# Optimization experiments

Hardware: AMD Instinct MI355X
Metric: run time of the kernel (lower is better)

## Reference

```python
import jax, jax.numpy as jnp
import numpy as np

E, T, DIN, DOUT = 8, 32768, 1024, 4096


def setup_inputs() -> dict:
    key = jax.random.key(0)
    k1, k2, k3 = jax.random.split(key, 3)
    input = jax.random.normal(k1, (T, DIN), dtype=jnp.float32)
    weight = jax.random.normal(k2, (E, DOUT, DIN), dtype=jnp.float32) * 0.02
    bias = jax.random.normal(k3, (E, DOUT), dtype=jnp.float32) * 0.02
    # balanced routing: 4096 tokens per expert, sums to T
    num_experts_per_token = jnp.full((E,), T // E, dtype=jnp.int64)
    return {"input": input, "weight": weight, "bias": bias,
            "num_experts_per_token": num_experts_per_token}


def reference(input, weight, bias, num_experts_per_token):
    # counts are routing metadata -> static (mirrors .tolist() in torch)
    counts = np.asarray(num_experts_per_token)
    offsets = np.concatenate([[0], np.cumsum(counts)])  # [E+1]
    num_experts = weight.shape[0]
    outs = []
    for i in range(num_experts):  # fixed small loop over experts (grouped GEMM)
        xi = input[offsets[i]:offsets[i + 1]]          # [n_i, DIN]
        yi = xi @ weight[i].T + bias[i]                # [n_i, DOUT]
        outs.append(yi)
    return jnp.concatenate(outs, axis=0)               # [T, DOUT]
```

## Files before the change

kernel.cpp:

```cpp
#include <hip/hip_runtime.h>
#include <hip/hip_bf16.h>


#define DEVFN __device__ __forceinline__

constexpr int E_    = 8;
constexpr int T_    = 32768;
constexpr int DIN_  = 1024;
constexpr int DOUT_ = 4096;

typedef __attribute__((ext_vector_type(8))) __bf16 bf16x8;
typedef __attribute__((ext_vector_type(4))) float  f32x4;
typedef __attribute__((ext_vector_type(8))) short  s16x8;

DEVFN unsigned short f2bf(float x) {
  unsigned u = __builtin_bit_cast(unsigned, x);
  u += 0x7fffu + ((u >> 16) & 1u);
  return (unsigned short)(u >> 16);
}

DEVFN long long expert_offset(const void* cnts, int e) {
  const int* c32 = (const int*)cnts;
  long long s = 0;
  for (int i = 0; i < E_; ++i) s += c32[i];
  if (s == (long long)T_) {
    long long o = 0;
    for (int i = 0; i < e; ++i) o += c32[i];
    return o;
  }
  const long long* c64 = (const long long*)cnts;
  long long o = 0;
  for (int i = 0; i < e; ++i) o += c64[i];
  return o;
}

__global__ __launch_bounds__(256) void cvt_kernel(const float* __restrict__ in,
                                                  unsigned short* __restrict__ out,
                                                  int n4) {
  int i = blockIdx.x * 256 + threadIdx.x;
  if (i >= n4) return;
  const float4 f = reinterpret_cast<const float4*>(in)[i];
  ushort4 h;
  h.x = f2bf(f.x); h.y = f2bf(f.y); h.z = f2bf(f.z); h.w = f2bf(f.w);
  reinterpret_cast<ushort4*>(out)[i] = h;
}

__global__ __launch_bounds__(512, 2) void gemm2_kernel(const unsigned short* __restrict__ wa,
                                                       const unsigned short* __restrict__ wb,
                                                       const float* __restrict__ bias,
                                                       const void* __restrict__ counts,
                                                       float* __restrict__ out) {
  __shared__ __align__(16) unsigned char lds[2][2][32768];

  const int tid  = threadIdx.x;
  const int lane = tid & 63;
  const int wid  = tid >> 6;
  const int wm = wid >> 2, wn = wid & 3;

  const int bid = blockIdx.x;
  const int sid = (bid & 7) * 256 + (bid >> 3);
  const int e  = sid >> 8;
  const int t  = sid & 255;
  const int tm = t >> 4, tn = t & 15;

  const long long off = expert_offset(counts, e);
  const unsigned short* wat = wa + (off + (long long)tm * 256) * DIN_;
  const unsigned short* wbt = wb + ((long long)(e * DOUT_ + tn * 256)) * DIN_;

  int goff[4], loff[4];
#pragma unroll
  for (int rd = 0; rd < 4; ++rd) {
    const int chunk = rd * 512 + tid;
    const int r = chunk >> 3, c = chunk & 7;
    goff[rd] = r * DIN_ + (c ^ (r & 7)) * 8;
    loff[rd] = chunk * 16;
  }
  auto stage = [&](const unsigned short* g, unsigned char* l) {
#pragma unroll
    for (int rd = 0; rd < 4; ++rd)
      __builtin_amdgcn_global_load_lds(
          (const __attribute__((address_space(1))) void*)(g + goff[rd]),
          (__attribute__((address_space(3))) void*)(l + loff[rd]), 16, 0, 0);
  };

  const int rsel = lane & 15, hi = lane >> 4;
  int lp[2];
  lp[0] = rsel * 128 + (((hi)     ^ (rsel & 7)) << 4);
  lp[1] = rsel * 128 + (((4 + hi) ^ (rsel & 7)) << 4);

  bf16x8 a[4][2];
  bf16x8 b[2][2][2];
  f32x4  acc[8][4] = {};

  auto quad = [&](int am0, int q) {
#pragma unroll
    for (int mf = 0; mf < 4; ++mf)
#pragma unroll
      for (int j = 0; j < 2; ++j)
#pragma unroll
        for (int kk = 0; kk < 2; ++kk)
          acc[am0 + mf][q * 2 + j] = __builtin_amdgcn_mfma_f32_16x16x32_bf16(
              a[mf][kk], b[q][j][kk], acc[am0 + mf][q * 2 + j], 0, 0, 0);
  };

  const int abase = wm * 128 * 128;
  const int bbase = wn * 64 * 128;

  auto ktile = [&](unsigned char* Ab, unsigned char* Bb,
                   const unsigned short* pfa, const unsigned short* pfb,
                   bool pf, int nend) {
#pragma unroll
    for (int mf = 0; mf < 4; ++mf)
#pragma unroll
      for (int kk = 0; kk < 2; ++kk)
        a[mf][kk] = *(const bf16x8*)(Ab + abase + mf * 2048 + lp[kk]);
#pragma unroll
    for (int j = 0; j < 2; ++j)
#pragma unroll
      for (int kk = 0; kk < 2; ++kk)
        b[0][j][kk] = *(const bf16x8*)(Bb + bbase + j * 2048 + lp[kk]);
    __builtin_amdgcn_s_barrier();
    asm volatile("s_waitcnt lgkmcnt(0)" ::: "memory");
    __builtin_amdgcn_sched_barrier(0);
    __builtin_amdgcn_s_setprio(1);
    quad(0, 0);
    __builtin_amdgcn_s_setprio(0);
    __builtin_amdgcn_s_barrier();

#pragma unroll
    for (int j = 0; j < 2; ++j)
#pragma unroll
      for (int kk = 0; kk < 2; ++kk)
        b[1][j][kk] = *(const bf16x8*)(Bb + bbase + (32 + j * 16) * 128 + lp[kk]);
    __builtin_amdgcn_s_barrier();
    asm volatile("s_waitcnt lgkmcnt(0)" ::: "memory");
    __builtin_amdgcn_sched_barrier(0);
    __builtin_amdgcn_s_setprio(1);
    quad(0, 1);
    __builtin_amdgcn_s_setprio(0);
    __builtin_amdgcn_s_barrier();

#pragma unroll
    for (int mf = 0; mf < 4; ++mf)
#pragma unroll
      for (int kk = 0; kk < 2; ++kk)
        a[mf][kk] = *(const bf16x8*)(Ab + abase + 8192 + mf * 2048 + lp[kk]);
    if (pf) stage(pfb, Bb);
    __builtin_amdgcn_s_barrier();
    asm volatile("s_waitcnt lgkmcnt(0)" ::: "memory");
    __builtin_amdgcn_sched_barrier(0);
    __builtin_amdgcn_s_setprio(1);
    quad(4, 1);
    __builtin_amdgcn_s_setprio(0);
    __builtin_amdgcn_s_barrier();

    if (pf) stage(pfa, Ab);
    __builtin_amdgcn_s_barrier();
    __builtin_amdgcn_sched_barrier(0);
    __builtin_amdgcn_s_setprio(1);
    quad(4, 0);
    __builtin_amdgcn_s_setprio(0);
    if (nend == 8)      asm volatile("s_waitcnt vmcnt(8)" ::: "memory");
    else if (nend == 0) asm volatile("s_waitcnt vmcnt(0)" ::: "memory");
    __builtin_amdgcn_s_barrier();
  };

  stage(wat,      &lds[0][0][0]);
  stage(wbt,      &lds[0][1][0]);
  stage(wat + 64, &lds[1][0][0]);
  stage(wbt + 64, &lds[1][1][0]);
  asm volatile("s_waitcnt vmcnt(8)" ::: "memory");
  __builtin_amdgcn_s_barrier();

  for (int it = 0; it < 7; ++it) {
    const int k0 = 2 * it;
    ktile(&lds[0][0][0], &lds[0][1][0], wat + (k0 + 2) * 64, wbt + (k0 + 2) * 64, true, 8);
    ktile(&lds[1][0][0], &lds[1][1][0], wat + (k0 + 3) * 64, wbt + (k0 + 3) * 64, true, 8);
  }
  ktile(&lds[0][0][0], &lds[0][1][0], nullptr, nullptr, false, 0);
  ktile(&lds[1][0][0], &lds[1][1][0], nullptr, nullptr, false, -1);

  const long long orow0 = off + (long long)tm * 256 + wm * 128;
  const int ocol0 = tn * 256 + wn * 64;
  const int rlo = hi * 4;
  const int c15 = rsel;
#pragma unroll
  for (int nf = 0; nf < 4; ++nf) {
    const int ncol = ocol0 + nf * 16 + c15;
    const float bv = bias[e * DOUT_ + ncol];
#pragma unroll
    for (int am = 0; am < 8; ++am) {
      const int rl = (am >> 2) * 64 + (am & 3) * 16 + rlo;
#pragma unroll
      for (int j = 0; j < 4; ++j)
        out[(orow0 + rl + j) * (long long)DOUT_ + ncol] = acc[am][nf][j] + bv;
    }
  }
}

__global__ __launch_bounds__(256) void gemm_fb_kernel(const float* __restrict__ Af,
                                                      const float* __restrict__ Bf,
                                                      const float* __restrict__ bias,
                                                      const void* __restrict__ counts,
                                                      float* __restrict__ out) {
  constexpr int RS = 144;
  constexpr int BBASE = 128 * RS;
  __shared__ __align__(16) unsigned char lds[2 * 128 * RS];

  const int tid  = threadIdx.x;
  const int lane = tid & 63;
  const int wid  = tid >> 6;
  const int wm = wid >> 1, wn = wid & 1;

  const int bid = blockIdx.x;
  const int e  = bid >> 10;
  const int t  = bid & 1023;
  const int tm = t >> 5, tn = t & 31;

  const long long off = expert_offset(counts, e);
  const long long rowA0 = off + (long long)tm * 128;
  const int n0 = tn * 128;

  f32x4 acc[4][4] = {};

  for (int kt = 0; kt < DIN_ / 64; ++kt) {
    const int k0 = kt * 64;
#pragma unroll
    for (int rd = 0; rd < 8; ++rd) {
      const int chunk = rd * 256 + tid;
      const int c2 = chunk & 1023;
      const int r  = c2 >> 3;
      const int c  = c2 & 7;
      const float* src =
          (rd < 4) ? (Af + (rowA0 + r) * (long long)DIN_ + (k0 + c * 8))
                   : (Bf + ((long long)(e * DOUT_ + n0 + r)) * DIN_ + (k0 + c * 8));
      const float4 f0 = *reinterpret_cast<const float4*>(src);
      const float4 f1 = *reinterpret_cast<const float4*>(src + 4);
      s16x8 v;
      v[0] = (short)f2bf(f0.x); v[1] = (short)f2bf(f0.y);
      v[2] = (short)f2bf(f0.z); v[3] = (short)f2bf(f0.w);
      v[4] = (short)f2bf(f1.x); v[5] = (short)f2bf(f1.y);
      v[6] = (short)f2bf(f1.z); v[7] = (short)f2bf(f1.w);
      *reinterpret_cast<s16x8*>(&lds[((rd < 4) ? 0 : BBASE) + r * RS + (c << 4)]) = v;
    }
    __syncthreads();
#pragma unroll
    for (int kk = 0; kk < 2; ++kk) {
      const int rs = lane & 15;
      const int cs = kk * 4 + (lane >> 4);
      bf16x8 af[4], bfr[4];
#pragma unroll
      for (int mf = 0; mf < 4; ++mf)
        af[mf] = *reinterpret_cast<const bf16x8*>(&lds[(wm * 64 + mf * 16 + rs) * RS + (cs << 4)]);
#pragma unroll
      for (int nf = 0; nf < 4; ++nf)
        bfr[nf] = *reinterpret_cast<const bf16x8*>(&lds[BBASE + (wn * 64 + nf * 16 + rs) * RS + (cs << 4)]);
#pragma unroll
      for (int mf = 0; mf < 4; ++mf)
#pragma unroll
        for (int nf = 0; nf < 4; ++nf)
          acc[mf][nf] = __builtin_amdgcn_mfma_f32_16x16x32_bf16(af[mf], bfr[nf], acc[mf][nf], 0, 0, 0);
    }
    __syncthreads();
  }

  const long long orow0 = off + (long long)tm * 128 + wm * 64;
  const int ocol0 = n0 + wn * 64;
  const int rlo = (lane >> 4) * 4;
  const int c15 = lane & 15;
#pragma unroll
  for (int nf = 0; nf < 4; ++nf) {
    const int n = ocol0 + nf * 16 + c15;
    const float bv = bias[e * DOUT_ + n];
#pragma unroll
    for (int mf = 0; mf < 4; ++mf) {
      const long long mrow = orow0 + mf * 16 + rlo;
#pragma unroll
      for (int j = 0; j < 4; ++j)
        out[(mrow + j) * (long long)DOUT_ + n] = acc[mf][nf][j] + bv;
    }
  }
}

extern "C" void kernel_launch(void* const* d_in, const int* in_sizes, int n_in,
                              void* d_out, int out_size, void* d_ws, size_t ws_size,
                              hipStream_t stream) {
  const float* input  = (const float*)d_in[0];
  const float* weight = (const float*)d_in[1];
  const float* bias   = (const float*)d_in[2];
  const void*  counts = (const void*)d_in[3];
  float* out = (float*)d_out;

  const size_t nA = (size_t)T_ * DIN_;
  const size_t nW = (size_t)E_ * DOUT_ * DIN_;
  const size_t need = (nA + nW) * sizeof(unsigned short);

  if (ws_size >= need) {
    unsigned short* wa = (unsigned short*)d_ws;
    unsigned short* wb = wa + nA;
    cvt_kernel<<<dim3((unsigned)(nA / 4 / 256)), dim3(256), 0, stream>>>(input, wa, (int)(nA / 4));
    cvt_kernel<<<dim3((unsigned)(nW / 4 / 256)), dim3(256), 0, stream>>>(weight, wb, (int)(nW / 4));
    gemm2_kernel<<<dim3(2048), dim3(512), 0, stream>>>(wa, wb, bias, counts, out);
  } else {
    gemm_fb_kernel<<<dim3(E_ * 32 * 32), dim3(256), 0, stream>>>(input, weight, bias, counts, out);
  }
}
```

Before: 403.8 us.

## Switch grouped GEMM to 256x128 tiles with BK=32 and 4-wave blocks

Replaces the 512-thread 256x256 tile kernel (BK=64, 128 KB LDS) with a 256-thread 256x128 tile kernel using BK=32 and 48 KB double-buffered LDS. The pipeline is restructured into per-k-tile phases that stage the next B tile and the A tile two steps ahead, with a new XOR swizzle for the narrower rows. This aims to raise occupancy and shorten the prologue and epilogue per block. In exchange the tile is smaller and k-steps shorter, so each block reuses less data and there are more barriers per unit of work.

```diff
diff --git a/kernel.cpp b/kernel.cpp
--- a/kernel.cpp
+++ b/kernel.cpp
@@ -8,6 +8,7 @@
 constexpr int T_    = 32768;
 constexpr int DIN_  = 1024;
 constexpr int DOUT_ = 4096;
+constexpr int NKT   = 32;
 
 typedef __attribute__((ext_vector_type(8))) __bf16 bf16x8;
 typedef __attribute__((ext_vector_type(4))) float  f32x4;
@@ -45,155 +46,124 @@
   reinterpret_cast<ushort4*>(out)[i] = h;
 }
 
-__global__ __launch_bounds__(512, 2) void gemm2_kernel(const unsigned short* __restrict__ wa,
+__global__ __launch_bounds__(256, 2) void gemm3_kernel(const unsigned short* __restrict__ wa,
                                                        const unsigned short* __restrict__ wb,
                                                        const float* __restrict__ bias,
                                                        const void* __restrict__ counts,
                                                        float* __restrict__ out) {
-  __shared__ __align__(16) unsigned char lds[2][2][32768];
+  __shared__ __align__(16) unsigned char lds[2][24576];
 
   const int tid  = threadIdx.x;
   const int lane = tid & 63;
   const int wid  = tid >> 6;
-  const int wm = wid >> 2, wn = wid & 3;
+  const int wm = wid >> 1, wn = wid & 1;
 
   const int bid = blockIdx.x;
-  const int sid = (bid & 7) * 256 + (bid >> 3);
-  const int e  = sid >> 8;
-  const int t  = sid & 255;
-  const int tm = t >> 4, tn = t & 15;
+  const int sid = (bid & 7) * 512 + (bid >> 3);
+  const int e  = sid >> 9;
+  const int t  = sid & 511;
+  const int tm = t >> 5, tn = t & 31;
 
   const long long off = expert_offset(counts, e);
   const unsigned short* wat = wa + (off + (long long)tm * 256) * DIN_;
-  const unsigned short* wbt = wb + ((long long)(e * DOUT_ + tn * 256)) * DIN_;
-
-  int goff[4], loff[4];
+  const unsigned short* wbt = wb + ((long long)(e * DOUT_ + tn * 128)) * DIN_;
+
+  int gA[4], gB[2];
 #pragma unroll
   for (int rd = 0; rd < 4; ++rd) {
-    const int chunk = rd * 512 + tid;
-    const int r = chunk >> 3, c = chunk & 7;
-    goff[rd] = r * DIN_ + (c ^ (r & 7)) * 8;
-    loff[rd] = chunk * 16;
-  }
-  auto stage = [&](const unsigned short* g, unsigned char* l) {
+    const int chunk = rd * 256 + tid;
+    const int r = chunk >> 2, c = chunk & 3;
+    gA[rd] = r * DIN_ + ((c ^ ((r >> 1) & 3)) << 3);
+  }
+#pragma unroll
+  for (int rd = 0; rd < 2; ++rd) {
+    const int chunk = rd * 256 + tid;
+    const int r = chunk >> 2, c = chunk & 3;
+    gB[rd] = r * DIN_ + ((c ^ ((r >> 1) & 3)) << 3);
+  }
+  auto stageA = [&](int kt, int buf) {
 #pragma unroll
     for (int rd = 0; rd < 4; ++rd)
       __builtin_amdgcn_global_load_lds(
-          (const __attribute__((address_space(1))) void*)(g + goff[rd]),
-          (__attribute__((address_space(3))) void*)(l + loff[rd]), 16, 0, 0);
+          (const __attribute__((address_space(1))) void*)(wat + kt * 32 + gA[rd]),
+          (__attribute__((address_space(3))) void*)(&lds[buf][(rd * 256 + tid) * 16]), 16, 0, 0);
   };
-
-  const int rsel = lane & 15, hi = lane >> 4;
-  int lp[2];
-  lp[0] = rsel * 128 + (((hi)     ^ (rsel & 7)) << 4);
-  lp[1] = rsel * 128 + (((4 + hi) ^ (rsel & 7)) << 4);
-
-  bf16x8 a[4][2];
-  bf16x8 b[2][2][2];
+  auto stageB = [&](int kt, int buf) {
+#pragma unroll
+    for (int rd = 0; rd < 2; ++rd)
+      __builtin_amdgcn_global_load_lds(
+          (const __attribute__((address_space(1))) void*)(wbt + kt * 32 + gB[rd]),
+          (__attribute__((address_space(3))) void*)(&lds[buf][16384 + (rd * 256 + tid) * 16]), 16, 0, 0);
+  };
+
+  const int rsel = lane & 15, g = lane >> 4;
+  const int swz = ((g ^ ((rsel >> 1) & 3)) << 4);
+  int laoff[8], lboff[4];
+#pragma unroll
+  for (int mf = 0; mf < 8; ++mf) laoff[mf] = (wm * 128 + mf * 16 + rsel) * 64 + swz;
+#pragma unroll
+  for (int nf = 0; nf < 4; ++nf) lboff[nf] = 16384 + (wn * 64 + nf * 16 + rsel) * 64 + swz;
+
+  bf16x8 a[8], b[2];
   f32x4  acc[8][4] = {};
 
-  auto quad = [&](int am0, int q) {
-#pragma unroll
-    for (int mf = 0; mf < 4; ++mf)
-#pragma unroll
-      for (int j = 0; j < 2; ++j)
-#pragma unroll
-        for (int kk = 0; kk < 2; ++kk)
-          acc[am0 + mf][q * 2 + j] = __builtin_amdgcn_mfma_f32_16x16x32_bf16(
-              a[mf][kk], b[q][j][kk], acc[am0 + mf][q * 2 + j], 0, 0, 0);
-  };
-
-  const int abase = wm * 128 * 128;
-  const int bbase = wn * 64 * 128;
-
-  auto ktile = [&](unsigned char* Ab, unsigned char* Bb,
-                   const unsigned short* pfa, const unsigned short* pfb,
-                   bool pf, int nend) {
-#pragma unroll
-    for (int mf = 0; mf < 4; ++mf)
-#pragma unroll
-      for (int kk = 0; kk < 2; ++kk)
-        a[mf][kk] = *(const bf16x8*)(Ab + abase + mf * 2048 + lp[kk]);
-#pragma unroll
-    for (int j = 0; j < 2; ++j)
-#pragma unroll
-      for (int kk = 0; kk < 2; ++kk)
-        b[0][j][kk] = *(const bf16x8*)(Bb + bbase + j * 2048 + lp[kk]);
+  stageA(0, 0);
+  stageB(0, 0);
+  stageA(1, 1);
+  asm volatile("s_waitcnt vmcnt(4)" ::: "memory");
+  __builtin_amdgcn_s_barrier();
+
+  for (int kt = 0; kt < NKT; ++kt) {
+    unsigned char* Ab = &lds[kt & 1][0];
+#pragma unroll
+    for (int mf = 0; mf < 8; ++mf) a[mf] = *(const bf16x8*)(Ab + laoff[mf]);
+    b[0] = *(const bf16x8*)(Ab + lboff[0]);
+    b[1] = *(const bf16x8*)(Ab + lboff[1]);
+    if (kt < NKT - 1) stageB(kt + 1, (kt + 1) & 1);
     __builtin_amdgcn_s_barrier();
     asm volatile("s_waitcnt lgkmcnt(0)" ::: "memory");
     __builtin_amdgcn_sched_barrier(0);
     __builtin_amdgcn_s_setprio(1);
-    quad(0, 0);
+#pragma unroll
+    for (int nf = 0; nf < 2; ++nf)
+#pragma unroll
+      for (int mf = 0; mf < 8; ++mf)
+        acc[mf][nf] = __builtin_amdgcn_mfma_f32_16x16x32_bf16(a[mf], b[nf], acc[mf][nf], 0, 0, 0);
     __builtin_amdgcn_s_setprio(0);
     __builtin_amdgcn_s_barrier();
 
-#pragma unroll
-    for (int j = 0; j < 2; ++j)
-#pragma unroll
-      for (int kk = 0; kk < 2; ++kk)
-        b[1][j][kk] = *(const bf16x8*)(Bb + bbase + (32 + j * 16) * 128 + lp[kk]);
+    b[0] = *(const bf16x8*)(Ab + lboff[2]);
+    b[1] = *(const bf16x8*)(Ab + lboff[3]);
+    if (kt < NKT - 2) stageA(kt + 2, kt & 1);
     __builtin_amdgcn_s_barrier();
     asm volatile("s_waitcnt lgkmcnt(0)" ::: "memory");
     __builtin_amdgcn_sched_barrier(0);
     __builtin_amdgcn_s_setprio(1);
-    quad(0, 1);
+#pragma unroll
+    for (int nf = 0; nf < 2; ++nf)
+#pragma unroll
+      for (int mf = 0; mf < 8; ++mf)
+        acc[mf][2 + nf] = __builtin_amdgcn_mfma_f32_16x16x32_bf16(a[mf], b[nf], acc[mf][2 + nf], 0, 0, 0);
     __builtin_amdgcn_s_setprio(0);
-    __builtin_amdgcn_s_barrier();
-
-#pragma unroll
-    for (int mf = 0; mf < 4; ++mf)
-#pragma unroll
-      for (int kk = 0; kk < 2; ++kk)
-        a[mf][kk] = *(const bf16x8*)(Ab + abase + 8192 + mf * 2048 + lp[kk]);
-    if (pf) stage(pfb, Bb);
-    __builtin_amdgcn_s_barrier();
-    asm volatile("s_waitcnt lgkmcnt(0)" ::: "memory");
-    __builtin_amdgcn_sched_barrier(0);
-    __builtin_amdgcn_s_setprio(1);
-    quad(4, 1);
-    __builtin_amdgcn_s_setprio(0);
-    __builtin_amdgcn_s_barrier();
-
-    if (pf) stage(pfa, Ab);
-    __builtin_amdgcn_s_barrier();
-    __builtin_amdgcn_sched_barrier(0);
-    __builtin_amdgcn_s_setprio(1);
-    quad(4, 0);
-    __builtin_amdgcn_s_setprio(0);
-    if (nend == 8)      asm volatile("s_waitcnt vmcnt(8)" ::: "memory");
-    else if (nend == 0) asm volatile("s_waitcnt vmcnt(0)" ::: "memory");
-    __builtin_amdgcn_s_barrier();
-  };
-
-  stage(wat,      &lds[0][0][0]);
-  stage(wbt,      &lds[0][1][0]);
-  stage(wat + 64, &lds[1][0][0]);
-  stage(wbt + 64, &lds[1][1][0]);
-  asm volatile("s_waitcnt vmcnt(8)" ::: "memory");
-  __builtin_amdgcn_s_barrier();
-
-  for (int it = 0; it < 7; ++it) {
-    const int k0 = 2 * it;
-    ktile(&lds[0][0][0], &lds[0][1][0], wat + (k0 + 2) * 64, wbt + (k0 + 2) * 64, true, 8);
-    ktile(&lds[1][0][0], &lds[1][1][0], wat + (k0 + 3) * 64, wbt + (k0 + 3) * 64, true, 8);
-  }
-  ktile(&lds[0][0][0], &lds[0][1][0], nullptr, nullptr, false, 0);
-  ktile(&lds[1][0][0], &lds[1][1][0], nullptr, nullptr, false, -1);
+    if (kt < NKT - 2)       asm volatile("s_waitcnt vmcnt(4)" ::: "memory");
+    else if (kt == NKT - 2) asm volatile("s_waitcnt vmcnt(0)" ::: "memory");
+    __builtin_amdgcn_s_barrier();
+  }
 
   const long long orow0 = off + (long long)tm * 256 + wm * 128;
-  const int ocol0 = tn * 256 + wn * 64;
-  const int rlo = hi * 4;
+  const int ocol0 = tn * 128 + wn * 64;
+  const int rlo = g * 4;
   const int c15 = rsel;
 #pragma unroll
   for (int nf = 0; nf < 4; ++nf) {
     const int ncol = ocol0 + nf * 16 + c15;
     const float bv = bias[e * DOUT_ + ncol];
 #pragma unroll
-    for (int am = 0; am < 8; ++am) {
-      const int rl = (am >> 2) * 64 + (am & 3) * 16 + rlo;
+    for (int mf = 0; mf < 8; ++mf) {
+      const long long mrow = orow0 + mf * 16 + rlo;
 #pragma unroll
       for (int j = 0; j < 4; ++j)
-        out[(orow0 + rl + j) * (long long)DOUT_ + ncol] = acc[am][nf][j] + bv;
+        out[(mrow + j) * (long long)DOUT_ + ncol] = acc[mf][nf][j] + bv;
     }
   }
 }
@@ -300,7 +270,7 @@
     unsigned short* wb = wa + nA;
     cvt_kernel<<<dim3((unsigned)(nA / 4 / 256)), dim3(256), 0, stream>>>(input, wa, (int)(nA / 4));
     cvt_kernel<<<dim3((unsigned)(nW / 4 / 256)), dim3(256), 0, stream>>>(weight, wb, (int)(nW / 4));
-    gemm2_kernel<<<dim3(2048), dim3(512), 0, stream>>>(wa, wb, bias, counts, out);
+    gemm3_kernel<<<dim3(4096), dim3(256), 0, stream>>>(wa, wb, bias, counts, out);
   } else {
     gemm_fb_kernel<<<dim3(E_ * 32 * 32), dim3(256), 0, stream>>>(input, weight, bias, counts, out);
   }
```

Result: slower. 461.9 us (+14.4%).

## Make GEMM persistent with 256 blocks and prefetch next tile across tile boundaries

Applied to the files above, without the earlier changes.

The grouped GEMM kernel becomes persistent. It launches 256 blocks, one per CU, and each block walks 8 output tiles of its expert. During the last k-steps of the current tile it prefetches the first k-tiles of the next tile, which hides the pipeline fill and drain between tiles. It also seeds the accumulators with the bias instead of adding it at store time, and removes some of the barriers and lgkmcnt waits inside the k-loop. The costs are a fixed tile assignment with no load balancing and possible LDS race risk from the reduced synchronisation.

```diff
diff --git a/kernel.cpp b/kernel.cpp
--- a/kernel.cpp
+++ b/kernel.cpp
@@ -45,7 +45,7 @@
   reinterpret_cast<ushort4*>(out)[i] = h;
 }
 
-__global__ __launch_bounds__(512, 2) void gemm2_kernel(const unsigned short* __restrict__ wa,
+__global__ __launch_bounds__(512, 2) void gemm4_kernel(const unsigned short* __restrict__ wa,
                                                        const unsigned short* __restrict__ wb,
                                                        const float* __restrict__ bias,
                                                        const void* __restrict__ counts,
@@ -57,114 +57,55 @@
   const int wid  = tid >> 6;
   const int wm = wid >> 2, wn = wid & 3;
 
-  const int bid = blockIdx.x;
-  const int sid = (bid & 7) * 256 + (bid >> 3);
-  const int e  = sid >> 8;
-  const int t  = sid & 255;
-  const int tm = t >> 4, tn = t & 15;
+  const int p = blockIdx.x;
+  const int e = p & 7;
+  const int q = p >> 3;
 
   const long long off = expert_offset(counts, e);
-  const unsigned short* wat = wa + (off + (long long)tm * 256) * DIN_;
-  const unsigned short* wbt = wb + ((long long)(e * DOUT_ + tn * 256)) * DIN_;
-
-  int goff[4], loff[4];
+  const unsigned short* wae = wa + off * (long long)DIN_;
+  const unsigned short* wbe = wb + (long long)e * DOUT_ * DIN_;
+  const float* be = bias + e * DOUT_;
+
+  int goff[4];
 #pragma unroll
   for (int rd = 0; rd < 4; ++rd) {
     const int chunk = rd * 512 + tid;
     const int r = chunk >> 3, c = chunk & 7;
-    goff[rd] = r * DIN_ + (c ^ (r & 7)) * 8;
-    loff[rd] = chunk * 16;
+    goff[rd] = r * DIN_ + ((c ^ (r & 7)) << 3);
   }
   auto stage = [&](const unsigned short* g, unsigned char* l) {
 #pragma unroll
     for (int rd = 0; rd < 4; ++rd)
       __builtin_amdgcn_global_load_lds(
           (const __attribute__((address_space(1))) void*)(g + goff[rd]),
-          (__attribute__((address_space(3))) void*)(l + loff[rd]), 16, 0, 0);
+          (__attribute__((address_space(3))) void*)(l + (rd * 512 + tid) * 16), 16, 0, 0);
   };
 
   const int rsel = lane & 15, hi = lane >> 4;
   int lp[2];
   lp[0] = rsel * 128 + (((hi)     ^ (rsel & 7)) << 4);
   lp[1] = rsel * 128 + (((4 + hi) ^ (rsel & 7)) << 4);
+  const int abase = wm * 128 * 128;
+  const int bbase = wn * 64 * 128;
 
   bf16x8 a[4][2];
   bf16x8 b[2][2][2];
-  f32x4  acc[8][4] = {};
-
-  auto quad = [&](int am0, int q) {
+  f32x4  acc[8][4];
+
+  auto quad = [&](int am0, int qn) {
 #pragma unroll
     for (int mf = 0; mf < 4; ++mf)
 #pragma unroll
       for (int j = 0; j < 2; ++j)
 #pragma unroll
         for (int kk = 0; kk < 2; ++kk)
-          acc[am0 + mf][q * 2 + j] = __builtin_amdgcn_mfma_f32_16x16x32_bf16(
-              a[mf][kk], b[q][j][kk], acc[am0 + mf][q * 2 + j], 0, 0, 0);
+          acc[am0 + mf][qn * 2 + j] = __builtin_amdgcn_mfma_f32_16x16x32_bf16(
+              a[mf][kk], b[qn][j][kk], acc[am0 + mf][qn * 2 + j], 0, 0, 0);
   };
 
-  const int abase = wm * 128 * 128;
-  const int bbase = wn * 64 * 128;
-
-  auto ktile = [&](unsigned char* Ab, unsigned char* Bb,
-                   const unsigned short* pfa, const unsigned short* pfb,
-                   bool pf, int nend) {
-#pragma unroll
-    for (int mf = 0; mf < 4; ++mf)
-#pragma unroll
-      for (int kk = 0; kk < 2; ++kk)
-        a[mf][kk] = *(const bf16x8*)(Ab + abase + mf * 2048 + lp[kk]);
-#pragma unroll
-    for (int j = 0; j < 2; ++j)
-#pragma unroll
-      for (int kk = 0; kk < 2; ++kk)
-        b[0][j][kk] = *(const bf16x8*)(Bb + bbase + j * 2048 + lp[kk]);
-    __builtin_amdgcn_s_barrier();
-    asm volatile("s_waitcnt lgkmcnt(0)" ::: "memory");
-    __builtin_amdgcn_sched_barrier(0);
-    __builtin_amdgcn_s_setprio(1);
-    quad(0, 0);
-    __builtin_amdgcn_s_setprio(0);
-    __builtin_amdgcn_s_barrier();
-
-#pragma unroll
-    for (int j = 0; j < 2; ++j)
-#pragma unroll
-      for (int kk = 0; kk < 2; ++kk)
-        b[1][j][kk] = *(const bf16x8*)(Bb + bbase + (32 + j * 16) * 128 + lp[kk]);
-    __builtin_amdgcn_s_barrier();
-    asm volatile("s_waitcnt lgkmcnt(0)" ::: "memory");
-    __builtin_amdgcn_sched_barrier(0);
-    __builtin_amdgcn_s_setprio(1);
-    quad(0, 1);
-    __builtin_amdgcn_s_setprio(0);
-    __builtin_amdgcn_s_barrier();
-
-#pragma unroll
-    for (int mf = 0; mf < 4; ++mf)
-#pragma unroll
-      for (int kk = 0; kk < 2; ++kk)
-        a[mf][kk] = *(const bf16x8*)(Ab + abase + 8192 + mf * 2048 + lp[kk]);
-    if (pf) stage(pfb, Bb);
-    __builtin_amdgcn_s_barrier();
-    asm volatile("s_waitcnt lgkmcnt(0)" ::: "memory");
-    __builtin_amdgcn_sched_barrier(0);
-    __builtin_amdgcn_s_setprio(1);
-    quad(4, 1);
-    __builtin_amdgcn_s_setprio(0);
-    __builtin_amdgcn_s_barrier();
-
-    if (pf) stage(pfa, Ab);
-    __builtin_amdgcn_s_barrier();
-    __builtin_amdgcn_sched_barrier(0);
-    __builtin_amdgcn_s_setprio(1);
-    quad(4, 0);
-    __builtin_amdgcn_s_setprio(0);
-    if (nend == 8)      asm volatile("s_waitcnt vmcnt(8)" ::: "memory");
-    else if (nend == 0) asm volatile("s_waitcnt vmcnt(0)" ::: "memory");
-    __builtin_amdgcn_s_barrier();
-  };
-
+  int tm = q >> 3, tn = q & 7;
+  const unsigned short* wat = wae + (long long)tm * 256 * DIN_;
+  const unsigned short* wbt = wbe + (long long)tn * 256 * DIN_;
   stage(wat,      &lds[0][0][0]);
   stage(wbt,      &lds[0][1][0]);
   stage(wat + 64, &lds[1][0][0]);
@@ -172,29 +113,84 @@
   asm volatile("s_waitcnt vmcnt(8)" ::: "memory");
   __builtin_amdgcn_s_barrier();
 
-  for (int it = 0; it < 7; ++it) {
-    const int k0 = 2 * it;
-    ktile(&lds[0][0][0], &lds[0][1][0], wat + (k0 + 2) * 64, wbt + (k0 + 2) * 64, true, 8);
-    ktile(&lds[1][0][0], &lds[1][1][0], wat + (k0 + 3) * 64, wbt + (k0 + 3) * 64, true, 8);
-  }
-  ktile(&lds[0][0][0], &lds[0][1][0], nullptr, nullptr, false, 0);
-  ktile(&lds[1][0][0], &lds[1][1][0], nullptr, nullptr, false, -1);
-
-  const long long orow0 = off + (long long)tm * 256 + wm * 128;
-  const int ocol0 = tn * 256 + wn * 64;
-  const int rlo = hi * 4;
-  const int c15 = rsel;
-#pragma unroll
-  for (int nf = 0; nf < 4; ++nf) {
-    const int ncol = ocol0 + nf * 16 + c15;
-    const float bv = bias[e * DOUT_ + ncol];
+  for (int it = 0; it < 8; ++it) {
+    const int ocol0 = tn * 256 + wn * 64;
+    {
+      const float bv0 = be[ocol0 + rsel];
+      const float bv1 = be[ocol0 + 16 + rsel];
+      const float bv2 = be[ocol0 + 32 + rsel];
+      const float bv3 = be[ocol0 + 48 + rsel];
+#pragma unroll
+      for (int am = 0; am < 8; ++am) {
+        acc[am][0] = (f32x4){bv0, bv0, bv0, bv0};
+        acc[am][1] = (f32x4){bv1, bv1, bv1, bv1};
+        acc[am][2] = (f32x4){bv2, bv2, bv2, bv2};
+        acc[am][3] = (f32x4){bv3, bv3, bv3, bv3};
+      }
+    }
+    const bool have_next = (it < 7);
+    int ntm = tm, ntn = tn;
+    if (have_next) { ntm = ((it + 1) & 3) * 4 + (q >> 3); ntn = ((it + 1) >> 2) * 8 + (q & 7); }
+    const unsigned short* nat = wae + (long long)ntm * 256 * DIN_;
+    const unsigned short* nbt = wbe + (long long)ntn * 256 * DIN_;
+
+    for (int kt = 0; kt < 16; ++kt) {
+      unsigned char* Ab = &lds[kt & 1][0][0];
+      unsigned char* Bb = &lds[kt & 1][1][0];
+      const unsigned short* pfa = nullptr;
+      const unsigned short* pfb = nullptr;
+      int nend = -1;
+      if (kt < 14)        { pfa = wat + (kt + 2) * 64; pfb = wbt + (kt + 2) * 64; nend = 8; }
+      else if (have_next) { pfa = nat + (kt - 14) * 64; pfb = nbt + (kt - 14) * 64; nend = 8; }
+      else if (kt == 14)  { nend = 0; }
+
+#pragma unroll
+      for (int mf = 0; mf < 4; ++mf) {
+        a[mf][0] = *(const bf16x8*)(Ab + abase + mf * 2048 + lp[0]);
+        a[mf][1] = *(const bf16x8*)(Ab + abase + mf * 2048 + lp[1]);
+      }
+#pragma unroll
+      for (int j = 0; j < 2; ++j) {
+        b[0][j][0] = *(const bf16x8*)(Bb + bbase + j * 2048 + lp[0]);
+        b[0][j][1] = *(const bf16x8*)(Bb + bbase + j * 2048 + lp[1]);
+      }
+      __builtin_amdgcn_s_setprio(1); quad(0, 0); __builtin_amdgcn_s_setprio(0);
+#pragma unroll
+      for (int j = 0; j < 2; ++j) {
+        b[1][j][0] = *(const bf16x8*)(Bb + bbase + 4096 + j * 2048 + lp[0]);
+        b[1][j][1] = *(const bf16x8*)(Bb + bbase + 4096 + j * 2048 + lp[1]);
+      }
+      __builtin_amdgcn_s_setprio(1); quad(0, 1); __builtin_amdgcn_s_setprio(0);
+      __builtin_amdgcn_s_barrier();
+      if (pfb) stage(pfb, Bb);
+#pragma unroll
+      for (int mf = 0; mf < 4; ++mf) {
+        a[mf][0] = *(const bf16x8*)(Ab + abase + 8192 + mf * 2048 + lp[0]);
+        a[mf][1] = *(const bf16x8*)(Ab + abase + 8192 + mf * 2048 + lp[1]);
+      }
+      __builtin_amdgcn_s_setprio(1); quad(4, 1); __builtin_amdgcn_s_setprio(0);
+      __builtin_amdgcn_s_barrier();
+      if (pfa) stage(pfa, Ab);
+      __builtin_amdgcn_s_setprio(1); quad(4, 0); __builtin_amdgcn_s_setprio(0);
+      if (nend == 8)      asm volatile("s_waitcnt vmcnt(8)" ::: "memory");
+      else if (nend == 0) asm volatile("s_waitcnt vmcnt(0)" ::: "memory");
+      __builtin_amdgcn_s_barrier();
+    }
+
+    const long long orow0 = off + (long long)tm * 256 + wm * 128;
 #pragma unroll
     for (int am = 0; am < 8; ++am) {
-      const int rl = (am >> 2) * 64 + (am & 3) * 16 + rlo;
-#pragma unroll
-      for (int j = 0; j < 4; ++j)
-        out[(orow0 + rl + j) * (long long)DOUT_ + ncol] = acc[am][nf][j] + bv;
-    }
+      const int rl = (am >> 2) * 64 + (am & 3) * 16 + hi * 4;
+#pragma unroll
+      for (int j = 0; j < 4; ++j) {
+        float* rp = out + (orow0 + rl + j) * (long long)DOUT_ + ocol0 + rsel;
+        rp[0]  = acc[am][0][j];
+        rp[16] = acc[am][1][j];
+        rp[32] = acc[am][2][j];
+        rp[48] = acc[am][3][j];
+      }
+    }
+    wat = nat; wbt = nbt; tm = ntm; tn = ntn;
   }
 }
 
@@ -300,7 +296,7 @@
     unsigned short* wb = wa + nA;
     cvt_kernel<<<dim3((unsigned)(nA / 4 / 256)), dim3(256), 0, stream>>>(input, wa, (int)(nA / 4));
     cvt_kernel<<<dim3((unsigned)(nW / 4 / 256)), dim3(256), 0, stream>>>(weight, wb, (int)(nW / 4));
-    gemm2_kernel<<<dim3(2048), dim3(512), 0, stream>>>(wa, wb, bias, counts, out);
+    gemm4_kernel<<<dim3(256), dim3(512), 0, stream>>>(wa, wb, bias, counts, out);
   } else {
     gemm_fb_kernel<<<dim3(E_ * 32 * 32), dim3(256), 0, stream>>>(input, weight, bias, counts, out);
   }
```

Result: faster. 369.9 us (-8.4%).
